# Kernel tuning notes

Measured on AMD Instinct MI355X. Metric: run time of the kernel, lower is better.

The kernel has to match this reference:

```python
import jax, jax.numpy as jnp
import numpy as np

D = 1024
H = 16
S = 2048
B = 4
DF = 4 * D
EPS = 1e-5


def setup_inputs() -> dict:
    key = jax.random.key(0)
    ks = jax.random.split(key, 12)
    sd = 0.02
    return {
        "x": jax.random.normal(ks[0], (B, S, D), dtype=jnp.float32),
        "Wq": jax.random.normal(ks[1], (D, D), dtype=jnp.float32) * sd,
        "Wk": jax.random.normal(ks[2], (D, D), dtype=jnp.float32) * sd,
        "Wv": jax.random.normal(ks[3], (D, D), dtype=jnp.float32) * sd,
        "Wo": jax.random.normal(ks[4], (D, D), dtype=jnp.float32) * sd,
        "bo": jnp.zeros((D,), dtype=jnp.float32),
        "W1": jax.random.normal(ks[5], (D, DF), dtype=jnp.float32) * sd,
        "b1": jnp.zeros((DF,), dtype=jnp.float32),
        "W2": jax.random.normal(ks[6], (DF, D), dtype=jnp.float32) * sd,
        "b2": jnp.zeros((D,), dtype=jnp.float32),
        "g1": jnp.ones((D,), dtype=jnp.float32),
        "s1": jnp.zeros((D,), dtype=jnp.float32),
        "g2": jnp.ones((D,), dtype=jnp.float32),
        "s2": jnp.zeros((D,), dtype=jnp.float32),
    }


def _gelu(x):
    # tanh approximation exactly as in the torch GELU module
    c = jnp.sqrt(jnp.asarray(2.0 / jnp.pi, dtype=x.dtype))
    return 0.5 * x * (1.0 + jnp.tanh(c * (x + 0.044715 * x ** 3)))


def _layernorm(x, scale, shift):
    mean = jnp.mean(x, axis=-1, keepdims=True)
    var = jnp.var(x, axis=-1, keepdims=True)  # biased, as unbiased=False
    return scale * (x - mean) * jax.lax.rsqrt(var + EPS) + shift


def _attention(x, Wq, Wk, Wv, Wo, bo):
    b, s, d = x.shape
    hd = d // H
    q = (x @ Wq).reshape(b, s, H, hd).transpose(0, 2, 1, 3)  # [b,h,s,hd]
    k = (x @ Wk).reshape(b, s, H, hd).transpose(0, 2, 1, 3)
    v = (x @ Wv).reshape(b, s, H, hd).transpose(0, 2, 1, 3)
    scores = jnp.einsum("bhqd,bhkd->bhqk", q, k) / jnp.sqrt(jnp.asarray(hd, x.dtype))
    mask = jnp.triu(jnp.ones((s, s), dtype=bool), k=1)
    scores = jnp.where(mask, -jnp.inf, scores)
    w = jax.nn.softmax(scores, axis=-1)  # dropout is identity (rate=0 / eval)
    ctx = jnp.einsum("bhqk,bhkd->bhqd", w, v)
    ctx = ctx.transpose(0, 2, 1, 3).reshape(b, s, d)
    return ctx @ Wo + bo


def reference(x, Wq, Wk, Wv, Wo, bo, W1, b1, W2, b2, g1, s1, g2, s2):
    h = x + _attention(_layernorm(x, g1, s1), Wq, Wk, Wv, Wo, bo)
    y = _layernorm(h, g2, s2)
    ff = _gelu(y @ W1 + b1) @ W2 + b2
    return h + ff
```

## Files before the change

### kernel.cpp

```cpp
#include <hip/hip_runtime.h>
#include <hip/hip_bf16.h>

#define DEV __device__ __forceinline__

typedef __bf16 bf16x8 __attribute__((ext_vector_type(8)));
typedef __bf16 bf16x2v __attribute__((ext_vector_type(2)));
typedef float f32x4 __attribute__((ext_vector_type(4)));
typedef float f32x16 __attribute__((ext_vector_type(16)));
typedef unsigned int u32;
typedef unsigned int u32x4 __attribute__((ext_vector_type(4)));
typedef __hip_bfloat16 hbf;

constexpr int Dm = 1024;
constexpr int Hh = 16;
constexpr int Ss = 2048;
constexpr int Bb = 4;
constexpr int DFm = 4096;
constexpr int LDQ = 3072;

DEV unsigned short f2bfu(float f) {
  hbf h = __float2bfloat16(f);
  return __builtin_bit_cast(unsigned short, h);
}

DEV float bfu2f(unsigned short u) { return __builtin_bit_cast(float, (u32)u << 16); }

DEV u32 pkbf(float x, float y) {
  bf16x2v v = {(__bf16)x, (__bf16)y};
  return __builtin_bit_cast(u32, v);
}

DEV float gelu_f(float x) {
  float e = __expf(-1.5957691216057308f * (x + 0.044715f * x * x * x));
  return x * __builtin_amdgcn_rcpf(1.f + e);
}

template <int N>
DEV void s_vmcnt() {
  if constexpr (N == 0) asm volatile("s_waitcnt vmcnt(0)" ::: "memory");
  else if constexpr (N == 5) asm volatile("s_waitcnt vmcnt(5)" ::: "memory");
  else if constexpr (N == 6) asm volatile("s_waitcnt vmcnt(6)" ::: "memory");
  else if constexpr (N == 8) asm volatile("s_waitcnt vmcnt(8)" ::: "memory");
  else static_assert(N == 0, "unsupported vmcnt");
}

#define GLDS(src, dst)                                                                     \
  __builtin_amdgcn_global_load_lds((const __attribute__((address_space(1))) void*)(src),   \
                                   (__attribute__((address_space(3))) void*)(dst), 16, 0, 0)

__global__ __launch_bounds__(256) void prep_kernel(
    const float* __restrict__ Wq, const float* __restrict__ Wk,
    const float* __restrict__ Wv, const float* __restrict__ Wo,
    const float* __restrict__ W1, const float* __restrict__ W2,
    hbf* __restrict__ dqkv, hbf* __restrict__ dwo,
    hbf* __restrict__ dw1, hbf* __restrict__ dw2,
    const float* __restrict__ x, const float* __restrict__ g1,
    const float* __restrict__ s1, hbf* __restrict__ xln) {
  const int i = blockIdx.x;
  if (i < 12288) {
    __shared__ float tile[32][33];
    const float* W;
    hbf* Wt;
    int K, N, k0, n0;
    if (i < 4096) {
      int z = i >> 10, j = i & 1023;
      W = z == 0 ? Wq : z == 1 ? Wk : z == 2 ? Wv : Wo;
      Wt = z == 3 ? dwo : dqkv + (size_t)z * 1024 * 1024;
      K = 1024; N = 1024; k0 = (j & 31) * 32; n0 = (j >> 5) * 32;
    } else if (i < 8192) {
      int j = i - 4096;
      W = W1; Wt = dw1; K = 1024; N = 4096;
      k0 = (j & 31) * 32; n0 = (j >> 5) * 32;
    } else {
      int j = i - 8192;
      W = W2; Wt = dw2; K = 4096; N = 1024;
      k0 = (j & 127) * 32; n0 = (j >> 7) * 32;
    }
    int tx = threadIdx.x & 31, ty = threadIdx.x >> 5;
    for (int r = ty; r < 32; r += 8) tile[r][tx] = W[(size_t)(k0 + r) * N + n0 + tx];
    __syncthreads();
    for (int r = ty; r < 32; r += 8)
      Wt[(size_t)(n0 + r) * K + k0 + tx] = __float2bfloat16(tile[tx][r]);
  } else {
    const int bid = i - 12288;
    int row = ((bid & 7) << 10) | (bid >> 3);
    int t = threadIdx.x;
    float4 v = ((const float4*)(x + (size_t)row * Dm))[t];
    float s = v.x + v.y + v.z + v.w;
    float q = v.x * v.x + v.y * v.y + v.z * v.z + v.w * v.w;
#pragma unroll
    for (int off = 32; off > 0; off >>= 1) {
      s += __shfl_down(s, off);
      q += __shfl_down(q, off);
    }
    __shared__ float red[10];
    int wave = t >> 6, lane = t & 63;
    if (lane == 0) { red[wave] = s; red[4 + wave] = q; }
    __syncthreads();
    if (t == 0) {
      float ts = red[0] + red[1] + red[2] + red[3];
      float tq = red[4] + red[5] + red[6] + red[7];
      float mean = ts * (1.f / Dm);
      float var = tq * (1.f / Dm) - mean * mean;
      red[8] = mean;
      red[9] = rsqrtf(var + 1e-5f);
    }
    __syncthreads();
    float mean = red[8], inv = red[9];
    float4 gv = ((const float4*)g1)[t];
    float4 bv = ((const float4*)s1)[t];
    ushort4 o;
    o.x = f2bfu(gv.x * (v.x - mean) * inv + bv.x);
    o.y = f2bfu(gv.y * (v.y - mean) * inv + bv.y);
    o.z = f2bfu(gv.z * (v.z - mean) * inv + bv.z);
    o.w = f2bfu(gv.w * (v.w - mean) * inv + bv.w);
    ((ushort4*)(xln + (size_t)row * Dm))[t] = o;
  }
}

__global__ __launch_bounds__(256) void ln_kernel(const hbf* __restrict__ xv,
                                                 const float* __restrict__ g,
                                                 const float* __restrict__ b,
                                                 hbf* __restrict__ y) {
  int row = ((blockIdx.x & 7) << 10) | (blockIdx.x >> 3);
  int t = threadIdx.x;
  float4 v;
  ushort4 u = ((const ushort4*)(xv + (size_t)row * Dm))[t];
  v.x = bfu2f(u.x); v.y = bfu2f(u.y); v.z = bfu2f(u.z); v.w = bfu2f(u.w);
  float s = v.x + v.y + v.z + v.w;
  float q = v.x * v.x + v.y * v.y + v.z * v.z + v.w * v.w;
#pragma unroll
  for (int off = 32; off > 0; off >>= 1) {
    s += __shfl_down(s, off);
    q += __shfl_down(q, off);
  }
  __shared__ float red[10];
  int wave = t >> 6, lane = t & 63;
  if (lane == 0) { red[wave] = s; red[4 + wave] = q; }
  __syncthreads();
  if (t == 0) {
    float ts = red[0] + red[1] + red[2] + red[3];
    float tq = red[4] + red[5] + red[6] + red[7];
    float mean = ts * (1.f / Dm);
    float var = tq * (1.f / Dm) - mean * mean;
    red[8] = mean;
    red[9] = rsqrtf(var + 1e-5f);
  }
  __syncthreads();
  float mean = red[8], inv = red[9];
  float4 gv = ((const float4*)g)[t];
  float4 bv = ((const float4*)b)[t];
  ushort4 o;
  o.x = f2bfu(gv.x * (v.x - mean) * inv + bv.x);
  o.y = f2bfu(gv.y * (v.y - mean) * inv + bv.y);
  o.z = f2bfu(gv.z * (v.z - mean) * inv + bv.z);
  o.w = f2bfu(gv.w * (v.w - mean) * inv + bv.w);
  ((ushort4*)(y + (size_t)row * Dm))[t] = o;
}

template <int BM, int BN, int WM, int WN, int NTHR, int NPH, int ACT, bool HAS_BIAS, int RES,
          bool OUT_BF16, int VTR>
__global__ __launch_bounds__(NTHR, 2) void gemm8(const hbf* __restrict__ A,
                                                 const hbf* __restrict__ Bt,
                                                 void* __restrict__ Cv,
                                                 const float* __restrict__ bias,
                                                 const void* __restrict__ resv,
                                                 hbf* __restrict__ vtrout,
                                                 int M, int N, int K) {
  constexpr int MR = (BM / WM) / 16, NR = (BN / WN) / 16;
  constexpr int MQ = MR / 2, NQ = NR / 2;
  constexpr int RPA = (BM / WM) / 2;
  constexpr int RPB = (BN / WN) / 2;
  constexpr int ASL = (BM / 2) * 64;
  constexpr int BSL = (BN / 2) * 64;
  constexpr int PERBUF = 2 * ASL + 2 * BSL;
  constexpr int ALD = ASL / (8 * NTHR);
  constexpr int BLD = BSL / (8 * NTHR);
  constexpr int VPB = 2 * ALD + BLD;
  constexpr int VP4 = 2 * ALD + 2 * BLD;

  __shared__ __align__(16) hbf lds[2 * PERBUF];

  const int tid = threadIdx.x;
  const int lane = tid & 63, wave = tid >> 6;
  const int wr = wave / WN, wc = wave % WN;
  const int lr = lane & 15, lg = lane >> 4;

  const int xcd = blockIdx.x & 7, oidx = blockIdx.x >> 3;
  const int gsup = oidx >> 6, r6 = oidx & 63;
  const int m0 = (xcd * 8 + (r6 >> 3)) * BM;
  const int n0 = (gsup * 8 + (r6 & 7)) * BN;

  const hbf* Ab = A + (size_t)m0 * K;
  const hbf* Bb = Bt + (size_t)n0 * K;

  f32x4 acc[MR][NR] = {};

  auto stageA = [&](int mh, int t, int p) {
#pragma unroll
    for (int l = 0; l < ALD; ++l) {
      int ci = l * NTHR + tid;
      int r = ci >> 3, c = ci & 7;
      int piece = r / RPA, rl = r % RPA;
      int grow = piece * (BM / WM) + mh * RPA + rl;
      int gk = t * 64 + ((c ^ (r & 7)) << 3);
      GLDS(Ab + (size_t)grow * K + gk, lds + p * PERBUF + mh * ASL + (size_t)ci * 8);
    }
  };
  auto stageB = [&](int nh, int t, int p) {
#pragma unroll
    for (int l = 0; l < BLD; ++l) {
      int ci = l * NTHR + tid;
      int r = ci >> 3, c = ci & 7;
      int piece = r / RPB, rl = r % RPB;
      int grow = piece * (BN / WN) + nh * RPB + rl;
      int gk = t * 64 + ((c ^ (r & 7)) << 3);
      GLDS(Bb + (size_t)grow * K + gk, lds + p * PERBUF + 2 * ASL + nh * BSL + (size_t)ci * 8);
    }
  };
  auto ldAfull = [&](bf16x8 (&af)[MR][2], int p) {
#pragma unroll
    for (int f = 0; f < MR; ++f)
#pragma unroll
      for (int ks = 0; ks < 2; ++ks) {
        int mh = f >> 1, i = f & 1;
        const hbf* base = lds + p * PERBUF + mh * ASL;
        int row = wr * RPA + i * 16 + lr;
        int slot = (ks * 4 + lg) ^ (lr & 7);
        af[f][ks] = *(const bf16x8*)(base + (size_t)row * 64 + slot * 8);
      }
  };
  auto ldA = [&](bf16x8 (&af)[MQ][2], int mh, int p) {
    const hbf* base = lds + p * PERBUF + mh * ASL;
#pragma unroll
    for (int i = 0; i < MQ; ++i)
#pragma unroll
      for (int ks = 0; ks < 2; ++ks) {
        int row = wr * RPA + i * 16 + lr;
        int slot = (ks * 4 + lg) ^ (lr & 7);
        af[i][ks] = *(const bf16x8*)(base + (size_t)row * 64 + slot * 8);
      }
  };
  auto ldB = [&](bf16x8 (&bf)[NQ][2], int nh, int p) {
    const hbf* base = lds + p * PERBUF + 2 * ASL + nh * BSL;
#pragma unroll
    for (int j = 0; j < NQ; ++j)
#pragma unroll
      for (int ks = 0; ks < 2; ++ks) {
        int row = wc * RPB + j * 16 + lr;
        int slot = (ks * 4 + lg) ^ (lr & 7);
        bf[j][ks] = *(const bf16x8*)(base + (size_t)row * 64 + slot * 8);
      }
  };

#define SYNC_LGKM()                                        \
  do {                                                     \
    __builtin_amdgcn_s_barrier();                          \
    asm volatile("s_waitcnt lgkmcnt(0)" ::: "memory");     \
    __builtin_amdgcn_sched_barrier(0);                     \
  } while (0)

#define MFMA_Q(av, bv, mh, nh)                                                        \
  do {                                                                                \
    __builtin_amdgcn_s_setprio(1);                                                    \
    _Pragma("unroll") for (int i_ = 0; i_ < MQ; ++i_)                                 \
    _Pragma("unroll") for (int j_ = 0; j_ < NQ; ++j_)                                 \
    _Pragma("unroll") for (int k_ = 0; k_ < 2; ++k_)                                  \
      acc[(mh) * MQ + i_][(nh) * NQ + j_] = __builtin_amdgcn_mfma_f32_16x16x32_bf16(  \
          (av)[i_][k_], (bv)[j_][k_], acc[(mh) * MQ + i_][(nh) * NQ + j_], 0, 0, 0);  \
    __builtin_amdgcn_s_setprio(0);                                                    \
  } while (0)

#define MFMA_H(av, bv, nh)                                                            \
  do {                                                                                \
    __builtin_amdgcn_s_setprio(1);                                                    \
    _Pragma("unroll") for (int f_ = 0; f_ < MR; ++f_)                                 \
    _Pragma("unroll") for (int j_ = 0; j_ < NQ; ++j_)                                 \
    _Pragma("unroll") for (int k_ = 0; k_ < 2; ++k_)                                  \
      acc[f_][(nh) * NQ + j_] = __builtin_amdgcn_mfma_f32_16x16x32_bf16(              \
          (av)[f_][k_], (bv)[j_][k_], acc[f_][(nh) * NQ + j_], 0, 0, 0);              \
    __builtin_amdgcn_s_setprio(0);                                                    \
  } while (0)

  const int T = K >> 6;

  if constexpr (NPH == 4) {
    stageA(0, 0, 0); stageB(0, 0, 0); stageA(1, 0, 0); stageB(1, 0, 0);
    stageA(0, 1, 1); stageB(0, 1, 1); stageA(1, 1, 1); stageB(1, 1, 1);
    s_vmcnt<VP4>();
    __builtin_amdgcn_s_barrier();

    for (int t = 0; t < T; ++t) {
      const int p = t & 1;
      bf16x8 a0[MQ][2], a1[MQ][2], b0[NQ][2], b1[NQ][2];
      ldA(a0, 0, p);
      ldB(b0, 0, p);
      asm volatile("s_waitcnt lgkmcnt(8)" ::: "memory");
      SYNC_LGKM();
      MFMA_Q(a0, b0, 0, 0);
      __builtin_amdgcn_s_barrier();
      ldA(a1, 1, p);
      if (t + 2 < T) { stageA(0, t + 2, p); stageB(0, t + 2, p); }
      SYNC_LGKM();
      MFMA_Q(a1, b0, 1, 0);
      __builtin_amdgcn_s_barrier();
      ldB(b1, 1, p);
      if (t + 2 < T) stageA(1, t + 2, p);
      SYNC_LGKM();
      MFMA_Q(a1, b1, 1, 1);
      __builtin_amdgcn_s_barrier();
      if (t + 2 < T) stageB(1, t + 2, p);
      MFMA_Q(a0, b1, 0, 1);
      if (t + 1 < T) {
        if (t + 2 < T) s_vmcnt<VP4>();
        else s_vmcnt<0>();
      }
      __builtin_amdgcn_s_barrier();
    }
  } else {
    stageA(0, 0, 0); stageA(1, 0, 0); stageB(0, 0, 0); stageB(1, 0, 0);
    stageA(0, 1, 1); stageA(1, 1, 1); stageB(0, 1, 1);
    s_vmcnt<VPB>();
    __builtin_amdgcn_s_barrier();

    for (int t = 0; t < T; ++t) {
      const int p = t & 1;
      bf16x8 af[MR][2], b0[NQ][2], b1[NQ][2];
      ldAfull(af, p);
      ldB(b0, 0, p);
      if (t + 1 < T) stageB(1, t + 1, p ^ 1);
      asm volatile("s_waitcnt lgkmcnt(8)" ::: "memory");
      SYNC_LGKM();
      MFMA_H(af, b0, 0);
      __builtin_amdgcn_s_barrier();
      ldB(b1, 1, p);
      if (t + 2 < T) { stageA(0, t + 2, p); stageA(1, t + 2, p); stageB(0, t + 2, p); }
      SYNC_LGKM();
      MFMA_H(af, b1, 1);
      if (t + 1 < T) {
        if (t + 2 < T) s_vmcnt<VPB>();
        else s_vmcnt<0>();
      }
      __builtin_amdgcn_s_barrier();
    }
  }
#undef SYNC_LGKM
#undef MFMA_Q
#undef MFMA_H

#pragma unroll
  for (int mf = 0; mf < MR; ++mf) {
    int row = m0 + wr * (BM / WM) + mf * 16 + lg * 4;
#pragma unroll
    for (int n = 0; n < NR; ++n) {
      int col = n0 + wc * (BN / WN) + n * 16 + lr;
      float bvl = HAS_BIAS ? bias[col] : 0.f;
      float tv[4];
#pragma unroll
      for (int j = 0; j < 4; ++j) {
        float v = acc[mf][n][j] + bvl;
        if (ACT == 1) v = gelu_f(v);
        if constexpr (RES == 1) v += ((const float*)resv)[(size_t)(row + j) * N + col];
        else if constexpr (RES == 2)
          v += bfu2f(__builtin_bit_cast(unsigned short,
                                        ((const hbf*)resv)[(size_t)(row + j) * N + col]));
        tv[j] = v;
      }
      if constexpr (VTR != 0) {
        if (col >= 2048) {
          ushort4 w;
          w.x = f2bfu(tv[0]); w.y = f2bfu(tv[1]); w.z = f2bfu(tv[2]); w.w = f2bfu(tv[3]);
          int bb = row >> 11;
          size_t vrow = (size_t)(bb * 1024 + col - 2048);
          *(ushort4*)((unsigned short*)vtrout + vrow * Ss + (row & 2047)) = w;
          continue;
        }
      }
#pragma unroll
      for (int j = 0; j < 4; ++j) {
        if (OUT_BF16) ((hbf*)Cv)[(size_t)(row + j) * N + col] = __float2bfloat16(tv[j]);
        else ((float*)Cv)[(size_t)(row + j) * N + col] = tv[j];
      }
    }
  }
}

__global__ __launch_bounds__(256, 4) void attn_kernel(const hbf* __restrict__ qkv,
                                                      const hbf* __restrict__ vt,
                                                      hbf* __restrict__ ctx) {
  __shared__ __align__(16) hbf Ks[2][64 * 64];
  __shared__ __align__(16) hbf Vs[2][64 * 64];

  const int tid = threadIdx.x;
  const int wave = tid >> 6, lane = tid & 63;
  const int l31 = lane & 31, hi = lane >> 5;

  const int gi = blockIdx.x;
  const int xslot = gi & 7, kk = gi >> 3;
  const int rank = kk >> 3, hg = kk & 7;
  const int bh = hg * 8 + xslot;
  const int bx = 15 - rank;
  const int b = bh >> 4, hh = bh & 15;
  const int q0b = bx * 128;
  const int q0w = q0b + wave * 32;
  const int nsteps = (q0b + 128) >> 6;
  const int my_steps = (q0w + 95) >> 6;

  constexpr float QSCALE = 0.18033688011112042f;
  bf16x8 qf[4];
  {
    const hbf* qrow = qkv + (size_t)(b * Ss + q0w + l31) * LDQ + hh * 64 + hi * 8;
#pragma unroll
    for (int ds = 0; ds < 4; ++ds) {
      bf16x8 t = *(const bf16x8*)(qrow + ds * 16);
#pragma unroll
      for (int e = 0; e < 8; ++e) qf[ds][e] = (__bf16)((float)t[e] * QSCALE);
    }
  }

  const hbf* kbase = qkv + 1024 + (size_t)(b * Ss) * LDQ + hh * 64;
  const hbf* vbase = vt + (size_t)(bh * 64) * Ss;
  const int i0 = tid, i1 = tid + 256;
  const int r0 = i0 >> 3, s0c = (i0 & 7), r1 = i1 >> 3, s1c = (i1 & 7);
  const int c0 = 8 * (s0c ^ (r0 & 7)), c1 = 8 * (s1c ^ (r1 & 7));

  f32x16 ot[2] = {};
  float m_run = -1e30f, l_run = 0.f;

  {
    hbf* kd = &Ks[0][0];
    hbf* vd = &Vs[0][0];
    GLDS(kbase + (size_t)r0 * LDQ + c0, kd + i0 * 8);
    GLDS(kbase + (size_t)r1 * LDQ + c1, kd + i1 * 8);
    GLDS(vbase + (size_t)r0 * Ss + c0, vd + i0 * 8);
    GLDS(vbase + (size_t)r1 * Ss + c1, vd + i1 * 8);
  }
  __syncthreads();

  int buf = 0;
  for (int it = 0; it < nsteps; ++it) {
    const int k0 = it << 6;
    if (it + 1 < nsteps) {
      hbf* kd = &Ks[buf ^ 1][0];
      hbf* vd = &Vs[buf ^ 1][0];
      GLDS(kbase + (size_t)(k0 + 64 + r0) * LDQ + c0, kd + i0 * 8);
      GLDS(kbase + (size_t)(k0 + 64 + r1) * LDQ + c1, kd + i1 * 8);
      GLDS(vbase + (size_t)r0 * Ss + k0 + 64 + c0, vd + i0 * 8);
      GLDS(vbase + (size_t)r1 * Ss + k0 + 64 + c1, vd + i1 * 8);
    }

    if (it < my_steps) {
      const hbf* kt = &Ks[buf][0];
      f32x16 st[2] = {};
      __builtin_amdgcn_s_setprio(1);
#pragma unroll
      for (int c = 0; c < 2; ++c) {
        const int krow = l31 + 32 * c;
        const int kr7 = krow & 7;
#pragma unroll
        for (int ds = 0; ds < 4; ++ds) {
          bf16x8 kf = *(const bf16x8*)(kt + krow * 64 + 8 * ((ds * 2 + hi) ^ kr7));
          st[c] = __builtin_amdgcn_mfma_f32_32x32x16_bf16(kf, qf[ds], st[c], 0, 0, 0);
        }
      }
      __builtin_amdgcn_s_setprio(0);

      if (it == my_steps - 1) {
        const int qg = q0w + l31;
#pragma unroll
        for (int c = 0; c < 2; ++c)
#pragma unroll
          for (int rg = 0; rg < 16; ++rg) {
            int kg = k0 + c * 32 + (rg & 3) + 8 * (rg >> 2) + 4 * hi;
            if (kg > qg) st[c][rg] = -3e38f;
          }
      }

      float mx = -3e38f;
#pragma unroll
      for (int c = 0; c < 2; ++c)
#pragma unroll
        for (int rg = 0; rg < 16; ++rg) mx = fmaxf(mx, st[c][rg]);
      mx = fmaxf(mx, __shfl_xor(mx, 32));
      if (!__all(mx - m_run <= 11.541560327111707f)) {
        float mn = fmaxf(m_run, mx);
        float sc = exp2f(m_run - mn);
        m_run = mn;
        l_run *= sc;
#pragma unroll
        for (int dc = 0; dc < 2; ++dc)
#pragma unroll
          for (int rg = 0; rg < 16; ++rg) ot[dc][rg] *= sc;
      }
      float rs = 0.f;
#pragma unroll
      for (int c = 0; c < 2; ++c)
#pragma unroll
        for (int rg = 0; rg < 16; ++rg) {
          float p = exp2f(st[c][rg] - m_run);
          st[c][rg] = p;
          rs += p;
        }
      rs += __shfl_xor(rs, 32);
      l_run += rs;

      bf16x8 pf[2][2];
#pragma unroll
      for (int c = 0; c < 2; ++c)
#pragma unroll
        for (int ks = 0; ks < 2; ++ks) {
          const int rb = ks * 8;
          u32 a0 = pkbf(st[c][rb + 0], st[c][rb + 1]);
          u32 a1 = pkbf(st[c][rb + 2], st[c][rb + 3]);
          u32 b0 = pkbf(st[c][rb + 4], st[c][rb + 5]);
          u32 b1 = pkbf(st[c][rb + 6], st[c][rb + 7]);
          u32 pa0 = __shfl_xor(a0, 32), pa1 = __shfl_xor(a1, 32);
          u32 pb0 = __shfl_xor(b0, 32), pb1 = __shfl_xor(b1, 32);
          u32x4 f;
          f.x = hi ? pb0 : a0;
          f.y = hi ? pb1 : a1;
          f.z = hi ? b0 : pa0;
          f.w = hi ? b1 : pa1;
          pf[c][ks] = __builtin_bit_cast(bf16x8, f);
        }

      const hbf* vtl = &Vs[buf][0];
      __builtin_amdgcn_s_setprio(1);
#pragma unroll
      for (int dc = 0; dc < 2; ++dc) {
        const int vrow = l31 + 32 * dc;
        const int vr7 = vrow & 7;
#pragma unroll
        for (int c = 0; c < 2; ++c)
#pragma unroll
          for (int ks = 0; ks < 2; ++ks) {
            bf16x8 vf = *(const bf16x8*)(vtl + vrow * 64 + 8 * ((c * 4 + ks * 2 + hi) ^ vr7));
            ot[dc] = __builtin_amdgcn_mfma_f32_32x32x16_bf16(vf, pf[c][ks], ot[dc], 0, 0, 0);
          }
      }
      __builtin_amdgcn_s_setprio(0);
    }

    __syncthreads();
    buf ^= 1;
  }

  const float inv = __builtin_amdgcn_rcpf(l_run);
  hbf* crow = ctx + (size_t)(b * Ss + q0w + l31) * Dm + hh * 64;
#pragma unroll
  for (int dc = 0; dc < 2; ++dc)
#pragma unroll
    for (int rg = 0; rg < 4; ++rg) {
      ushort4 w;
      w.x = f2bfu(ot[dc][rg * 4 + 0] * inv);
      w.y = f2bfu(ot[dc][rg * 4 + 1] * inv);
      w.z = f2bfu(ot[dc][rg * 4 + 2] * inv);
      w.w = f2bfu(ot[dc][rg * 4 + 3] * inv);
      *(ushort4*)(crow + dc * 32 + rg * 8 + hi * 4) = w;
    }
}

extern "C" void kernel_launch(void* const* d_in, const int* in_sizes, int n_in,
                              void* d_out, int out_size, void* d_ws, size_t ws_size,
                              hipStream_t stream) {
  const float* x  = (const float*)d_in[0];
  const float* Wq = (const float*)d_in[1];
  const float* Wk = (const float*)d_in[2];
  const float* Wv = (const float*)d_in[3];
  const float* Wo = (const float*)d_in[4];
  const float* bo = (const float*)d_in[5];
  const float* W1 = (const float*)d_in[6];
  const float* b1 = (const float*)d_in[7];
  const float* W2 = (const float*)d_in[8];
  const float* b2 = (const float*)d_in[9];
  const float* g1 = (const float*)d_in[10];
  const float* s1 = (const float*)d_in[11];
  const float* g2 = (const float*)d_in[12];
  const float* s2 = (const float*)d_in[13];
  float* out = (float*)d_out;

  char* ws = (char*)d_ws;
  constexpr size_t MB = 1024ull * 1024ull;
  hbf* wqkvT = (hbf*)(ws + 0 * MB);
  hbf* woT   = (hbf*)(ws + 6 * MB);
  hbf* w1T   = (hbf*)(ws + 8 * MB);
  hbf* w2T   = (hbf*)(ws + 16 * MB);
  hbf* xln   = (hbf*)(ws + 24 * MB);
  hbf* ctx   = (hbf*)(ws + 24 * MB);
  hbf* y2    = (hbf*)(ws + 24 * MB);
  hbf* qkvb  = (hbf*)(ws + 40 * MB);
  hbf* vtb   = (hbf*)(ws + 88 * MB);
  hbf* ff1   = (hbf*)(ws + 40 * MB);
  hbf* hbb   = (hbf*)(ws + 104 * MB);
  (void)ws_size; (void)in_sizes; (void)n_in; (void)out_size;

  const int BS = Bb * Ss;

  prep_kernel<<<20480, 256, 0, stream>>>(Wq, Wk, Wv, Wo, W1, W2,
                                         wqkvT, woT, w1T, w2T, x, g1, s1, xln);

  gemm8<128, 128, 2, 2, 256, 2, 0, false, 0, true, 1><<<1536, 256, 0, stream>>>(
      xln, wqkvT, qkvb, nullptr, nullptr, vtb, BS, LDQ, Dm);

  attn_kernel<<<dim3(1024), 256, 0, stream>>>(qkvb, vtb, ctx);

  gemm8<128, 128, 2, 2, 256, 2, 0, true, 1, true, 0><<<512, 256, 0, stream>>>(
      ctx, woT, hbb, bo, x, nullptr, BS, Dm, Dm);

  ln_kernel<<<BS, 256, 0, stream>>>(hbb, g2, s2, y2);

  gemm8<128, 128, 2, 2, 256, 2, 1, true, 0, true, 0><<<2048, 256, 0, stream>>>(
      y2, w1T, ff1, b1, nullptr, nullptr, BS, DFm, Dm);

  gemm8<128, 128, 2, 2, 256, 2, 0, true, 2, false, 0><<<512, 256, 0, stream>>>(
      ff1, w2T, out, b2, hbb, nullptr, BS, Dm, DFm);
}
```

Baseline: 335.1 us.

## Simplify GEMM main loop to single-phase prefetch with one barrier pair per K-tile

Removes the unused 4-phase GEMM path and reworks the 2-phase loop. Each K-tile now does all LDS fragment reads up front, waits once, runs every MFMA, and then issues the whole next-next tile's global-to-LDS loads together. Previously the loads were interleaved between MFMA halves with extra barriers. The aim is fewer barriers and less waitcnt overhead per tile. In exchange, global loads overlap less with MFMA work inside a tile, and register pressure rises because both B halves are held at once.

```diff
diff --git a/kernel.cpp b/kernel.cpp
--- a/kernel.cpp
+++ b/kernel.cpp
@@ -158,7 +158,7 @@
   ((ushort4*)(y + (size_t)row * Dm))[t] = o;
 }
 
-template <int BM, int BN, int WM, int WN, int NTHR, int NPH, int ACT, bool HAS_BIAS, int RES,
+template <int BM, int BN, int WM, int WN, int NTHR, int ACT, bool HAS_BIAS, int RES,
           bool OUT_BF16, int VTR>
 __global__ __launch_bounds__(NTHR, 2) void gemm8(const hbf* __restrict__ A,
                                                  const hbf* __restrict__ Bt,
@@ -168,7 +168,7 @@
                                                  hbf* __restrict__ vtrout,
                                                  int M, int N, int K) {
   constexpr int MR = (BM / WM) / 16, NR = (BN / WN) / 16;
-  constexpr int MQ = MR / 2, NQ = NR / 2;
+  constexpr int NQ = NR / 2;
   constexpr int RPA = (BM / WM) / 2;
   constexpr int RPB = (BN / WN) / 2;
   constexpr int ASL = (BM / 2) * 64;
@@ -176,8 +176,8 @@
   constexpr int PERBUF = 2 * ASL + 2 * BSL;
   constexpr int ALD = ASL / (8 * NTHR);
   constexpr int BLD = BSL / (8 * NTHR);
-  constexpr int VPB = 2 * ALD + BLD;
-  constexpr int VP4 = 2 * ALD + 2 * BLD;
+  constexpr int LPT = 2 * ALD + 2 * BLD;
+  static_assert(LPT == 8, "vmcnt constant assumes 8 loads/K-tile");
 
   __shared__ __align__(16) hbf lds[2 * PERBUF];
 
@@ -230,17 +230,6 @@
         af[f][ks] = *(const bf16x8*)(base + (size_t)row * 64 + slot * 8);
       }
   };
-  auto ldA = [&](bf16x8 (&af)[MQ][2], int mh, int p) {
-    const hbf* base = lds + p * PERBUF + mh * ASL;
-#pragma unroll
-    for (int i = 0; i < MQ; ++i)
-#pragma unroll
-      for (int ks = 0; ks < 2; ++ks) {
-        int row = wr * RPA + i * 16 + lr;
-        int slot = (ks * 4 + lg) ^ (lr & 7);
-        af[i][ks] = *(const bf16x8*)(base + (size_t)row * 64 + slot * 8);
-      }
-  };
   auto ldB = [&](bf16x8 (&bf)[NQ][2], int nh, int p) {
     const hbf* base = lds + p * PERBUF + 2 * ASL + nh * BSL;
 #pragma unroll
@@ -252,24 +241,6 @@
         bf[j][ks] = *(const bf16x8*)(base + (size_t)row * 64 + slot * 8);
       }
   };
-
-#define SYNC_LGKM()                                        \
-  do {                                                     \
-    __builtin_amdgcn_s_barrier();                          \
-    asm volatile("s_waitcnt lgkmcnt(0)" ::: "memory");     \
-    __builtin_amdgcn_sched_barrier(0);                     \
-  } while (0)
-
-#define MFMA_Q(av, bv, mh, nh)                                                        \
-  do {                                                                                \
-    __builtin_amdgcn_s_setprio(1);                                                    \
-    _Pragma("unroll") for (int i_ = 0; i_ < MQ; ++i_)                                 \
-    _Pragma("unroll") for (int j_ = 0; j_ < NQ; ++j_)                                 \
-    _Pragma("unroll") for (int k_ = 0; k_ < 2; ++k_)                                  \
-      acc[(mh) * MQ + i_][(nh) * NQ + j_] = __builtin_amdgcn_mfma_f32_16x16x32_bf16(  \
-          (av)[i_][k_], (bv)[j_][k_], acc[(mh) * MQ + i_][(nh) * NQ + j_], 0, 0, 0);  \
-    __builtin_amdgcn_s_setprio(0);                                                    \
-  } while (0)
 
 #define MFMA_H(av, bv, nh)                                                            \
   do {                                                                                \
@@ -284,68 +255,32 @@
 
   const int T = K >> 6;
 
-  if constexpr (NPH == 4) {
-    stageA(0, 0, 0); stageB(0, 0, 0); stageA(1, 0, 0); stageB(1, 0, 0);
-    stageA(0, 1, 1); stageB(0, 1, 1); stageA(1, 1, 1); stageB(1, 1, 1);
-    s_vmcnt<VP4>();
+  stageA(0, 0, 0); stageA(1, 0, 0); stageB(0, 0, 0); stageB(1, 0, 0);
+  stageA(0, 1, 1); stageA(1, 1, 1); stageB(0, 1, 1); stageB(1, 1, 1);
+  s_vmcnt<8>();
+  __builtin_amdgcn_s_barrier();
+
+  for (int t = 0; t < T; ++t) {
+    const int p = t & 1;
+    bf16x8 af[MR][2], b0[NQ][2], b1[NQ][2];
+    ldAfull(af, p);
+    ldB(b0, 0, p);
+    ldB(b1, 1, p);
+    asm volatile("s_waitcnt lgkmcnt(0)" ::: "memory");
+    __builtin_amdgcn_sched_barrier(0);
+    MFMA_H(af, b0, 0);
+    MFMA_H(af, b1, 1);
     __builtin_amdgcn_s_barrier();
-
-    for (int t = 0; t < T; ++t) {
-      const int p = t & 1;
-      bf16x8 a0[MQ][2], a1[MQ][2], b0[NQ][2], b1[NQ][2];
-      ldA(a0, 0, p);
-      ldB(b0, 0, p);
-      asm volatile("s_waitcnt lgkmcnt(8)" ::: "memory");
-      SYNC_LGKM();
-      MFMA_Q(a0, b0, 0, 0);
+    if (t + 2 < T) {
+      stageA(0, t + 2, p); stageA(1, t + 2, p);
+      stageB(0, t + 2, p); stageB(1, t + 2, p);
+    }
+    if (t + 1 < T) {
+      if (t + 2 < T) s_vmcnt<8>();
+      else s_vmcnt<0>();
       __builtin_amdgcn_s_barrier();
-      ldA(a1, 1, p);
-      if (t + 2 < T) { stageA(0, t + 2, p); stageB(0, t + 2, p); }
-      SYNC_LGKM();
-      MFMA_Q(a1, b0, 1, 0);
-      __builtin_amdgcn_s_barrier();
-      ldB(b1, 1, p);
-      if (t + 2 < T) stageA(1, t + 2, p);
-      SYNC_LGKM();
-      MFMA_Q(a1, b1, 1, 1);
-      __builtin_amdgcn_s_barrier();
-      if (t + 2 < T) stageB(1, t + 2, p);
-      MFMA_Q(a0, b1, 0, 1);
-      if (t + 1 < T) {
-        if (t + 2 < T) s_vmcnt<VP4>();
-        else s_vmcnt<0>();
-      }
-      __builtin_amdgcn_s_barrier();
-    }
-  } else {
-    stageA(0, 0, 0); stageA(1, 0, 0); stageB(0, 0, 0); stageB(1, 0, 0);
-    stageA(0, 1, 1); stageA(1, 1, 1); stageB(0, 1, 1);
-    s_vmcnt<VPB>();
-    __builtin_amdgcn_s_barrier();
-
-    for (int t = 0; t < T; ++t) {
-      const int p = t & 1;
-      bf16x8 af[MR][2], b0[NQ][2], b1[NQ][2];
-      ldAfull(af, p);
-      ldB(b0, 0, p);
-      if (t + 1 < T) stageB(1, t + 1, p ^ 1);
-      asm volatile("s_waitcnt lgkmcnt(8)" ::: "memory");
-      SYNC_LGKM();
-      MFMA_H(af, b0, 0);
-      __builtin_amdgcn_s_barrier();
-      ldB(b1, 1, p);
-      if (t + 2 < T) { stageA(0, t + 2, p); stageA(1, t + 2, p); stageB(0, t + 2, p); }
-      SYNC_LGKM();
-      MFMA_H(af, b1, 1);
-      if (t + 1 < T) {
-        if (t + 2 < T) s_vmcnt<VPB>();
-        else s_vmcnt<0>();
-      }
-      __builtin_amdgcn_s_barrier();
-    }
-  }
-#undef SYNC_LGKM
-#undef MFMA_Q
+    }
+  }
 #undef MFMA_H
 
 #pragma unroll
@@ -599,19 +534,19 @@
   prep_kernel<<<20480, 256, 0, stream>>>(Wq, Wk, Wv, Wo, W1, W2,
                                          wqkvT, woT, w1T, w2T, x, g1, s1, xln);
 
-  gemm8<128, 128, 2, 2, 256, 2, 0, false, 0, true, 1><<<1536, 256, 0, stream>>>(
+  gemm8<128, 128, 2, 2, 256, 0, false, 0, true, 1><<<1536, 256, 0, stream>>>(
       xln, wqkvT, qkvb, nullptr, nullptr, vtb, BS, LDQ, Dm);
 
   attn_kernel<<<dim3(1024), 256, 0, stream>>>(qkvb, vtb, ctx);
 
-  gemm8<128, 128, 2, 2, 256, 2, 0, true, 1, true, 0><<<512, 256, 0, stream>>>(
+  gemm8<128, 128, 2, 2, 256, 0, true, 1, true, 0><<<512, 256, 0, stream>>>(
       ctx, woT, hbb, bo, x, nullptr, BS, Dm, Dm);
 
   ln_kernel<<<BS, 256, 0, stream>>>(hbb, g2, s2, y2);
 
-  gemm8<128, 128, 2, 2, 256, 2, 1, true, 0, true, 0><<<2048, 256, 0, stream>>>(
+  gemm8<128, 128, 2, 2, 256, 1, true, 0, true, 0><<<2048, 256, 0, stream>>>(
       y2, w1T, ff1, b1, nullptr, nullptr, BS, DFm, Dm);
 
-  gemm8<128, 128, 2, 2, 256, 2, 0, true, 2, false, 0><<<512, 256, 0, stream>>>(
+  gemm8<128, 128, 2, 2, 256, 0, true, 2, false, 0><<<512, 256, 0, stream>>>(
       ff1, w2T, out, b2, hbb, nullptr, BS, Dm, DFm);
 }
```

Result: no change. 336.9 us (+0.5%).
